# Optimization experiments

Measured on AMD Instinct MI355X. Metric: run time of the kernel, lower is better.

The kernel has to match this reference:

```python
import jax, jax.numpy as jnp
import numpy as np

B, N, D = 4, 2048, 256
EPS = 1e-5


def _clinear(Z, W, b):
    # complex linear: Z (B,2,N,din), W (2,dout,din), b (2,dout)
    Zr, Zi = Z[:, 0], Z[:, 1]
    Wr, Wi = W[0], W[1]
    outr = Zr @ Wr.T - Zi @ Wi.T + b[0]
    outi = Zr @ Wi.T + Zi @ Wr.T + b[1]
    return jnp.stack([outr, outi], axis=1)


def setup_inputs() -> dict:
    key = jax.random.key(0)
    ks = jax.random.split(key, 14)
    sc = 1.0 / np.sqrt(D).astype(np.float32)
    t = jnp.tile(jnp.arange(N + 1, dtype=jnp.float32)[None] * 0.01, (B, 1))
    return {
        'Z_q': jax.random.normal(ks[0], (B, 2, N, D), jnp.float32),
        'Z_k': jax.random.normal(ks[1], (B, 2, N, D), jnp.float32),
        'Z_v': jax.random.normal(ks[2], (B, 2, N, D), jnp.float32),
        't_measure_all': t,
        'W_q': jax.random.normal(ks[3], (2, D, D), jnp.float32) * sc,
        'b_q': jax.random.normal(ks[4], (2, D), jnp.float32) * 0.01,
        'W_k': jax.random.normal(ks[5], (2, D, D), jnp.float32) * sc,
        'b_k': jax.random.normal(ks[6], (2, D), jnp.float32) * 0.01,
        'W_v': jax.random.normal(ks[7], (2, D, D), jnp.float32) * sc,
        'b_v': jax.random.normal(ks[8], (2, D), jnp.float32) * 0.01,
        'W_p': jax.random.normal(ks[9], (2, D, D), jnp.float32) * sc,
        'b_p': jax.random.normal(ks[10], (2, D), jnp.float32) * 0.01,
        'lambda1': jax.random.normal(ks[11], (2, D // 2, 1), jnp.float32),
        'lambda_Omega_sqrt': jax.random.normal(ks[12], (1, D, 1), jnp.float32) * sc,
        'lambda_Gamma_sqrt': jax.random.normal(ks[13], (1, D, 1), jnp.float32) * sc,
        'tau': jnp.asarray(1.0, jnp.float32),
        'delta': jnp.asarray(0.0, jnp.float32),
        'lambda_C': jnp.ones((1, D, 1), jnp.float32),
    }


def reference(Z_q, Z_k, Z_v, t_measure_all, W_q, b_q, W_k, b_k, W_v, b_v,
              W_p, b_p, lambda1, lambda_Omega_sqrt, lambda_Gamma_sqrt,
              tau, delta, lambda_C):
    # lambda_h = 0 * compute_lambda_h(lambda1): conjugate-pair spectrum, zeroed in forward
    lam_r = 0.0 * jnp.concatenate([lambda1[0], lambda1[0]], axis=0)[:, 0]   # (D,)
    lam_i = 0.0 * jnp.concatenate([lambda1[1], -lambda1[1]], axis=0)[:, 0]  # (D,)
    lam_Om = lambda_Omega_sqrt ** 2 + EPS   # process noise (1,D,1)
    lam_Ga = lambda_Gamma_sqrt ** 2 + EPS   # measurement noise (1,D,1)

    Q = _clinear(Z_q, W_q, b_q)  # (B,2,N,D)
    K = _clinear(Z_k, W_k, b_k)
    V = _clinear(Z_v, W_v, b_v)

    t = t_measure_all[0, :-1]  # (N,)
    # exponential state-transition kernels exp(+/- lambda * t): (2,N,D)
    mag_f = jnp.exp(lam_r[None] * t[:, None]); ph_f = lam_i[None] * t[:, None]
    exp_f = jnp.stack([mag_f * jnp.cos(ph_f), mag_f * jnp.sin(ph_f)])
    mag_b = jnp.exp(-lam_r[None] * t[:, None]); ph_b = -lam_i[None] * t[:, None]
    exp_b = jnp.stack([mag_b * jnp.cos(ph_b), mag_b * jnp.sin(ph_b)])
    # one-step transition exp(lambda * dt): (2,D)
    dt = t[1] - t[0]
    mat_exp = jnp.stack([jnp.exp(lam_r * dt) * jnp.cos(lam_i * dt),
                         jnp.exp(lam_r * dt) * jnp.sin(lam_i * dt)])

    # averaged covariance kernel, exact lambda->0 limit: Gamma + Omega*|t_i-t_j|, mean over D
    lamC2 = lambda_C[0, :, 0] ** 2
    ga_bar = jnp.mean(lamC2 * lam_Ga[0, :, 0])
    om_bar = jnp.mean(lamC2 * lam_Om[0, :, 0])
    abs_dt = jnp.abs(t[:, None] - t[None, :])          # (N,N)
    V_avg_ij = ga_bar + om_bar * abs_dt                # (N,N)

    # factorized kernels
    V_v = exp_f[None]                 # (1,2,N,D)
    U_q = exp_b[None] * Q             # (B,2,N,D)
    U_k = exp_b[None] * K
    U_v = exp_b[None] * V

    # precision-weighted squared residual norm R_ij = sum_d |V_k|^2 |U_q_i - U_k_j|^2
    Vk_abs = jnp.sum(exp_f ** 2, axis=0)              # (N,D)
    Uk_abs = jnp.sum(U_k ** 2, axis=1)                # (B,N,D)
    Uq_abs = jnp.sum(U_q ** 2, axis=1)                # (B,N,D)
    T1 = jnp.einsum('id,bjd->bij', Vk_abs, Uk_abs)
    T2 = jnp.sum(Vk_abs[None] * Uq_abs, axis=2)[:, :, None]
    T3 = (jnp.einsum('bid,bjd->bij', Vk_abs[None] * U_q[:, 0], U_k[:, 0]) +
          jnp.einsum('bid,bjd->bij', Vk_abs[None] * U_q[:, 1], U_k[:, 1]))
    R_qk_abs = T1 + T2 - 2.0 * T3                     # (B,N,N)

    scores = -(tau ** 2) * jnp.log(V_avg_ij[None] + R_qk_abs)
    mask = jnp.tril(jnp.ones((N, N), bool))
    scores = jnp.where(mask[None], scores, -jnp.inf)
    A = jax.nn.softmax(scores, axis=2)                # (B,N,N)
    Q_ij = jnp.stack([A, jnp.zeros_like(A)], axis=1)  # (B,2,N,N)

    # est_inner = complex matmul(Q_ij, U_v); Q imag part is zero
    est_inner = jnp.stack([jnp.einsum('bij,bjd->bid', A, U_v[:, 0]),
                           jnp.einsum('bij,bjd->bid', A, U_v[:, 1])], axis=1)
    est_v = V_v * est_inner          # plain elementwise product, as in source
    s = jax.nn.sigmoid(delta)
    est_eigenbasis = (1.0 - s) * V + s * est_v        # (B,2,N,D)

    # complex Hadamard with one-step transition
    pr = mat_exp[0][None, None] * est_eigenbasis[:, 0] - mat_exp[1][None, None] * est_eigenbasis[:, 1]
    pi = mat_exp[0][None, None] * est_eigenbasis[:, 1] + mat_exp[1][None, None] * est_eigenbasis[:, 0]
    pred_p = jnp.stack([pr, pi], axis=1)
    out = _clinear(pred_p, W_p, b_p)                  # (B,2,N,D)

    lambda_h = jnp.stack([lam_r, lam_i])[..., None]
    return est_eigenbasis, out, Q_ij, V_v, U_v, lambda_h
```

## Files before the change

### kernel.cpp

```cpp
#include <hip/hip_runtime.h>
#include <math.h>

#define BN 4
#define NN 2048
#define DD 256
#define EPSF 1e-5f

typedef __attribute__((ext_vector_type(8))) short bf16x8;
typedef __attribute__((ext_vector_type(4))) float f32x4;

constexpr size_t OFF_EST = 0;
constexpr size_t OFF_OUT = (size_t)BN * 2 * NN * DD;
constexpr size_t OFF_QIJ = OFF_OUT + (size_t)BN * 2 * NN * DD;
constexpr size_t OFF_VV  = OFF_QIJ + (size_t)BN * 2 * NN * NN;
constexpr size_t OFF_UV  = OFF_VV + (size_t)2 * NN * DD;
constexpr size_t OFF_LH  = OFF_UV + (size_t)BN * 2 * NN * DD;

constexpr size_t SCR_B0   = OFF_QIJ + (size_t)NN * NN;
constexpr size_t U_Q16    = 0;
constexpr size_t U_K16    = (size_t)BN * NN * DD;
constexpr size_t U_VT16   = 2 * (size_t)BN * NN * DD;
constexpr size_t SCR_QN   = SCR_B0 + 3 * (size_t)BN * NN * DD / 2;
constexpr size_t SCR_KN   = SCR_QN + (size_t)BN * NN;
constexpr size_t SCR_L    = SCR_KN + (size_t)BN * NN;
constexpr size_t SCR_SC   = SCR_L + (size_t)BN * NN;
constexpr size_t SCR_W16P = SCR_SC + 16;
constexpr size_t SCR_E16F = OFF_QIJ + 3 * (size_t)NN * NN;
constexpr size_t U_PART   = (size_t)BN * NN * 512;
constexpr size_t SCR_Z16F = OFF_QIJ + 5 * (size_t)NN * NN;
constexpr size_t SCR_Z16VF = OFF_QIJ + 7 * (size_t)NN * NN;
constexpr size_t U_W16    = (size_t)BN * NN * 512;
constexpr size_t W16_PER_B = 136 * 16384;

__device__ __forceinline__ short f2bf(float x) {
    union { float f; unsigned u; } v; v.f = x;
    unsigned r = v.u + 0x7fff + ((v.u >> 16) & 1);
    return (short)(r >> 16);
}
__device__ __forceinline__ float bf2f(unsigned short h) {
    union { unsigned u; float f; } v; v.u = ((unsigned)h) << 16;
    return v.f;
}
__device__ __forceinline__ unsigned short* u16p(float* d, size_t fofs) {
    return (unsigned short*)(d + fofs);
}
__device__ __forceinline__ const unsigned short* u16pc(const float* d, size_t fofs) {
    return (const unsigned short*)(d + fofs);
}
__device__ __forceinline__ unsigned short* w16p(float* d, int b) {
    return (b < 3) ? u16p(d, SCR_Z16F) + (size_t)b * W16_PER_B
                   : u16p(d, SCR_Z16VF);
}
__device__ __forceinline__ const unsigned short* w16pc(const float* d, int b) {
    return (b < 3) ? u16pc(d, SCR_Z16F) + (size_t)b * W16_PER_B
                   : u16pc(d, SCR_Z16VF);
}
__device__ __forceinline__ int nc_of(int TI) { return TI >= 12 ? 3 : (TI >= 6 ? 2 : 1); }
__device__ __forceinline__ int cb_of(int TI) {
    return TI < 6 ? TI : (TI < 12 ? 6 + 2 * (TI - 6) : 18 + 3 * (TI - 12));
}

__device__ __forceinline__ void gll16(const unsigned short* g, short* l) {
    __builtin_amdgcn_global_load_lds(
        (const __attribute__((address_space(1))) unsigned*)g,
        (__attribute__((address_space(3))) unsigned*)l, 16, 0, 0);
}
__device__ __forceinline__ void stage_tile(const unsigned short* gbase, size_t stride_sh,
                                           short* ldsbuf, int t) {
    const int w = t >> 6, L = t & 63;
#pragma unroll
    for (int p = 0; p < 2; ++p) {
        const int r0 = w * 32 + p * 16;
        const unsigned short* src = gbase + (size_t)(r0 + (L >> 2)) * stride_sh + (L & 3) * 8;
        gll16(src, ldsbuf + r0 * 32);
    }
}
__device__ __forceinline__ void stage64(const unsigned short* gbase, size_t stride_sh,
                                        short* ldsbuf, int t) {
    const int w = t >> 6, L = t & 63;
    const int r0 = w * 16;
    const unsigned short* src = gbase + (size_t)(r0 + (L >> 2)) * stride_sh + (L & 3) * 8;
    gll16(src, ldsbuf + r0 * 32);
}

__global__ void k_cvt(const float* __restrict__ Zq, const float* __restrict__ Zk,
                      const float* __restrict__ Zv,
                      const float* __restrict__ Wq, const float* __restrict__ Wk,
                      const float* __restrict__ Wv, const float* __restrict__ Wp,
                      const float* __restrict__ tau, const float* __restrict__ delta,
                      const float* __restrict__ lamOm, const float* __restrict__ lamGa,
                      const float* __restrict__ lamC,
                      float* __restrict__ dout) {
    const int z = blockIdx.z;
    if (z < 3) {
        const float* Z = (z == 0) ? Zq : (z == 1) ? Zk : Zv;
        unsigned short* O = (z == 0) ? u16p(dout, SCR_Z16F)
                          : (z == 1) ? u16p(dout, SCR_Z16F) + (size_t)BN * NN * 512
                                     : u16p(dout, SCR_Z16VF);
        const long n4 = (long)BN * 2 * NN * DD / 4;
        for (long i4 = (long)blockIdx.x * 256 + threadIdx.x; i4 < n4;
             i4 += (long)gridDim.x * 256) {
            const long i = i4 * 4;
            const int d = (int)(i & (DD - 1));
            const long r = i >> 8;
            const int n = (int)(r & (NN - 1));
            const long bc = r >> 11;
            const int c = (int)(bc & 1), b = (int)(bc >> 1);
            float4 v = *(const float4*)&Z[i];
            ushort4 o;
            o.x = (unsigned short)f2bf(v.x); o.y = (unsigned short)f2bf(v.y);
            o.z = (unsigned short)f2bf(v.z); o.w = (unsigned short)f2bf(v.w);
            *(ushort4*)&O[((size_t)(b * NN + n)) * 512 + c * 256 + d] = o;
        }
    } else if (z == 3) {
        const float* Ws[4] = {Wq, Wk, Wv, Wp};
        const long n4 = 6L * 256 * 512 / 4;
        for (long e4 = (long)blockIdx.x * 256 + threadIdx.x; e4 < n4;
             e4 += (long)gridDim.x * 256) {
            const long e = e4 * 4;
            const int k = (int)(e & 511);
            const long rest = e >> 9;
            const int dd = (int)(rest & 255);
            const int m = (int)(rest >> 8);
            int proj, mode;
            if (m < 3)      { proj = m; mode = 0; }
            else if (m == 3){ proj = 2; mode = 1; }
            else            { proj = 3; mode = m - 4; }
            const int kc = k >> 8, kk = k & 255;
            int wc; float sgn;
            if (mode == 0) { wc = kc; sgn = kc ? -1.f : 1.f; }
            else           { wc = 1 - kc; sgn = 1.f; }
            float4 v = *(const float4*)&Ws[proj][((size_t)wc * DD + dd) * DD + kk];
            ushort4 o;
            o.x = (unsigned short)f2bf(sgn * v.x); o.y = (unsigned short)f2bf(sgn * v.y);
            o.z = (unsigned short)f2bf(sgn * v.z); o.w = (unsigned short)f2bf(sgn * v.w);
            unsigned short* dst = (m < 4)
                ? u16p(dout, SCR_Z16VF) + U_W16 + (size_t)m * 131072
                : u16p(dout, SCR_W16P) + (size_t)(m - 4) * 131072;
            *(ushort4*)&dst[(size_t)dd * 512 + k] = o;
        }
    } else {
        const int idx = blockIdx.x * 256 + threadIdx.x;
        if (idx < 3 * BN * NN) dout[SCR_QN + idx] = 0.f;
        if (blockIdx.x == 0) {
            __shared__ float red[8];
            const int t = threadIdx.x;
            float c2 = lamC[t] * lamC[t];
            float ga = c2 * (lamGa[t] * lamGa[t] + EPSF);
            float om = c2 * (lamOm[t] * lamOm[t] + EPSF);
            for (int o = 32; o > 0; o >>= 1) {
                ga += __shfl_down(ga, o, 64);
                om += __shfl_down(om, o, 64);
            }
            if ((t & 63) == 0) { red[t >> 6] = ga; red[4 + (t >> 6)] = om; }
            __syncthreads();
            if (t == 0) {
                float gs = red[0] + red[1] + red[2] + red[3];
                float os = red[4] + red[5] + red[6] + red[7];
                float* scal = dout + SCR_SC;
                scal[0] = tau[0] * tau[0];
                scal[1] = 1.f / (1.f + __expf(-delta[0]));
                scal[2] = gs / 256.f;
                scal[3] = os / 256.f;
            }
        }
    }
}

__global__ __launch_bounds__(256) void k_qkv(const float* __restrict__ bq,
                                             const float* __restrict__ bk,
                                             const float* __restrict__ bv,
                                             float* __restrict__ dout)
{
    __shared__ short Al[64 * 32];
    __shared__ short Bl[128 * 32];
    const int z = blockIdx.z;
    const int d0 = blockIdx.x * 128;
    const int b = blockIdx.y >> 5;
    const int n0 = (blockIdx.y & 31) * 64;

    const unsigned short* Z16 =
        (z == 0) ? u16pc(dout, SCR_Z16F)
      : (z == 1) ? u16pc(dout, SCR_Z16F) + (size_t)BN * NN * 512
                 : u16pc(dout, SCR_Z16VF);
    const unsigned short* W16 = u16pc(dout, SCR_Z16VF) + U_W16 + (size_t)z * 131072;
    const float* bias = (z == 0) ? bq : (z == 1) ? bk : bv;
    const int bofs = (z == 3) ? DD : 0;

    const int t = threadIdx.x, wave = t >> 6, lane = t & 63, quad = lane >> 4, lm = lane & 15;
    const int wr = (wave >> 1) * 32, wc = (wave & 1) * 64;
    const unsigned short* Abase = Z16 + (size_t)(b * NN + n0) * 512;
    const unsigned short* Bbase = W16 + (size_t)d0 * 512;

    f32x4 acc[2][4];
#pragma unroll
    for (int i = 0; i < 2; ++i)
#pragma unroll
        for (int j = 0; j < 4; ++j) acc[i][j] = (f32x4){0.f, 0.f, 0.f, 0.f};

    for (int kt = 0; kt < 16; ++kt) {
        const int kk0 = kt * 32;
        stage64(Abase + kk0, 512, Al, t);
        stage_tile(Bbase + kk0, 512, Bl, t);
        __syncthreads();
        bf16x8 af[2], bff[4];
#pragma unroll
        for (int mi = 0; mi < 2; ++mi) af[mi] = *(const bf16x8*)&Al[(wr + mi * 16 + lm) * 32 + quad * 8];
#pragma unroll
        for (int nj = 0; nj < 4; ++nj) bff[nj] = *(const bf16x8*)&Bl[(wc + nj * 16 + lm) * 32 + quad * 8];
#pragma unroll
        for (int mi = 0; mi < 2; ++mi)
#pragma unroll
            for (int nj = 0; nj < 4; ++nj)
                acc[mi][nj] = __builtin_amdgcn_mfma_f32_16x16x32_bf16(af[mi], bff[nj], acc[mi][nj], 0, 0, 0);
        __syncthreads();
    }

    if (z <= 1) {
        unsigned short* O16 = u16p(dout, SCR_B0) + (z ? U_K16 : U_Q16) + (size_t)b * NN * DD;
        float* NRM = dout + (z ? SCR_KN : SCR_QN) + b * NN;
#pragma unroll
        for (int mi = 0; mi < 2; ++mi)
#pragma unroll
            for (int r = 0; r < 4; ++r) {
                const int m = n0 + wr + mi * 16 + quad * 4 + r;
                float ss = 0.f;
#pragma unroll
                for (int nj = 0; nj < 4; ++nj) {
                    const int d = d0 + wc + nj * 16 + lm;
                    unsigned short h = (unsigned short)f2bf(acc[mi][nj][r] + bias[d]);
                    O16[(size_t)m * DD + d] = h;
                    const float vb = bf2f(h);
                    ss = fmaf(vb, vb, ss);
                }
                ss += __shfl_down(ss, 8, 16); ss += __shfl_down(ss, 4, 16);
                ss += __shfl_down(ss, 2, 16); ss += __shfl_down(ss, 1, 16);
                if (lm == 0) atomicAdd(&NRM[m], ss);
            }
    } else if (z == 2) {
        float* UV0 = dout + OFF_UV + (size_t)(b * 2) * NN * DD;
#pragma unroll
        for (int mi = 0; mi < 2; ++mi)
#pragma unroll
            for (int r = 0; r < 4; ++r) {
                const int m = n0 + wr + mi * 16 + quad * 4 + r;
#pragma unroll
                for (int nj = 0; nj < 4; ++nj) {
                    const int d = d0 + wc + nj * 16 + lm;
                    UV0[(size_t)m * DD + d] = acc[mi][nj][r] + bias[d];
                }
            }
    } else {
        const float s1 = 1.f - dout[SCR_SC + 1];
        float* EST1 = dout + OFF_EST + (size_t)(b * 2 + 1) * NN * DD;
        unsigned short* E16 = u16p(dout, SCR_E16F) + (size_t)b * NN * 512;
#pragma unroll
        for (int mi = 0; mi < 2; ++mi)
#pragma unroll
            for (int r = 0; r < 4; ++r) {
                const int m = n0 + wr + mi * 16 + quad * 4 + r;
#pragma unroll
                for (int nj = 0; nj < 4; ++nj) {
                    const int d = d0 + wc + nj * 16 + lm;
                    const float v = s1 * (acc[mi][nj][r] + bias[bofs + d]);
                    EST1[(size_t)m * DD + d] = v;
                    E16[(size_t)m * 512 + 256 + d] = (unsigned short)f2bf(v);
                }
            }
    }
}

__global__ __launch_bounds__(256) void k_outproj(const float* __restrict__ bp,
                                                 float* __restrict__ dout)
{
    __shared__ short Al[64 * 32];
    __shared__ short Bl[128 * 32];
    const int z = blockIdx.z;
    if (z == 2) {
        const long idx = (long)(blockIdx.y * 2 + blockIdx.x) * 256 + threadIdx.x;
        const float4 zz4 = {0.f, 0.f, 0.f, 0.f};
        for (long u = idx * 4; u < (long)NN * NN; u += 256L * 256 * 4) {
            *(float4*)&dout[SCR_Z16F + u] = zz4;
            *(float4*)&dout[SCR_Z16VF + u] = zz4;
        }
        return;
    }
    const int d0 = blockIdx.x * 128;
    const int b = blockIdx.y >> 5;
    const int n0 = (blockIdx.y & 31) * 64;
    const unsigned short* E16 = u16pc(dout, SCR_E16F) + (size_t)b * NN * 512;
    const unsigned short* W16 = u16pc(dout, SCR_W16P) + (size_t)z * 131072;

    const int t = threadIdx.x, wave = t >> 6, lane = t & 63, quad = lane >> 4, lm = lane & 15;
    const int wr = (wave >> 1) * 32, wc = (wave & 1) * 64;
    const unsigned short* Abase = E16 + (size_t)n0 * 512;
    const unsigned short* Bbase = W16 + (size_t)d0 * 512;

    f32x4 acc[2][4];
#pragma unroll
    for (int i = 0; i < 2; ++i)
#pragma unroll
        for (int j = 0; j < 4; ++j) acc[i][j] = (f32x4){0.f, 0.f, 0.f, 0.f};

    for (int kt = 0; kt < 16; ++kt) {
        const int kk0 = kt * 32;
        stage64(Abase + kk0, 512, Al, t);
        stage_tile(Bbase + kk0, 512, Bl, t);
        __syncthreads();
        bf16x8 af[2], bff[4];
#pragma unroll
        for (int mi = 0; mi < 2; ++mi) af[mi] = *(const bf16x8*)&Al[(wr + mi * 16 + lm) * 32 + quad * 8];
#pragma unroll
        for (int nj = 0; nj < 4; ++nj) bff[nj] = *(const bf16x8*)&Bl[(wc + nj * 16 + lm) * 32 + quad * 8];
#pragma unroll
        for (int mi = 0; mi < 2; ++mi)
#pragma unroll
            for (int nj = 0; nj < 4; ++nj)
                acc[mi][nj] = __builtin_amdgcn_mfma_f32_16x16x32_bf16(af[mi], bff[nj], acc[mi][nj], 0, 0, 0);
        __syncthreads();
    }
    const int bofs = z ? DD : 0;
    float* O = dout + OFF_OUT + (size_t)(b * 2 + z) * NN * DD;
#pragma unroll
    for (int mi = 0; mi < 2; ++mi)
#pragma unroll
        for (int r = 0; r < 4; ++r) {
            const int m = n0 + wr + mi * 16 + quad * 4 + r;
#pragma unroll
            for (int nj = 0; nj < 4; ++nj) {
                const int d = d0 + wc + nj * 16 + lm;
                O[(size_t)m * DD + d] = acc[mi][nj][r] + bp[bofs + d];
            }
        }
}

__global__ __launch_bounds__(256) void k_scores(const float* __restrict__ tmeas,
                                                float* __restrict__ dout) {
    __shared__ __align__(16) float smemf[4160];
    short* Al = (short*)smemf;
    short* Bl = ((short*)smemf) + 2048;
    const int b = blockIdx.y;
    if (blockIdx.x >= 272) {
        float (*T)[65] = (float(*)[65])smemf;
        const int vj = blockIdx.x - 272;
        const int nb = (vj & 31) * 64, db = (vj >> 5) * 64;
        const float* V = dout + OFF_UV + (size_t)(b * 2) * NN * DD;
        unsigned short* VT = u16p(dout, SCR_B0) + U_VT16 + (size_t)b * DD * NN;
        const int tr = threadIdx.x >> 4, tc = (threadIdx.x & 15) * 4;
#pragma unroll
        for (int p = 0; p < 4; ++p) {
            float4 v = *(const float4*)&V[(size_t)(nb + tr + p * 16) * DD + db + tc];
            T[tr + p * 16][tc + 0] = v.x; T[tr + p * 16][tc + 1] = v.y;
            T[tr + p * 16][tc + 2] = v.z; T[tr + p * 16][tc + 3] = v.w;
        }
        __syncthreads();
#pragma unroll
        for (int p = 0; p < 4; ++p) {
            const int d = tr + p * 16;
            ushort4 o;
            o.x = (unsigned short)f2bf(T[tc + 0][d]);
            o.y = (unsigned short)f2bf(T[tc + 1][d]);
            o.z = (unsigned short)f2bf(T[tc + 2][d]);
            o.w = (unsigned short)f2bf(T[tc + 3][d]);
            *(ushort4*)&VT[(size_t)(db + d) * NN + nb + tc] = o;
        }
        return;
    }
    const int x2 = blockIdx.x;
    const int x = x2 >> 1, ih = x2 & 1;
    int ti = (int)((sqrtf(8.f * x + 1.f) - 1.f) * 0.5f);
    while ((ti + 1) * (ti + 2) / 2 <= x) ++ti;
    while (ti * (ti + 1) / 2 > x) --ti;
    const int tj = x - ti * (ti + 1) / 2;
    const int i0 = ti * 128, j0 = tj * 128;
    const int ib = i0 + ih * 64;
    const unsigned short* Q16 = u16pc(dout, SCR_B0) + U_Q16 + (size_t)b * NN * DD;
    const unsigned short* K16 = u16pc(dout, SCR_B0) + U_K16 + (size_t)b * NN * DD;
    const int t = threadIdx.x, wave = t >> 6, lane = t & 63, quad = lane >> 4, lm = lane & 15;
    const int wr = (wave >> 1) * 32, wc = (wave & 1) * 64;
    const unsigned short* Abase = Q16 + (size_t)ib * DD;
    const unsigned short* Bbase = K16 + (size_t)j0 * DD;

    f32x4 acc[2][4];
#pragma unroll
    for (int i = 0; i < 2; ++i)
#pragma unroll
        for (int j = 0; j < 4; ++j) acc[i][j] = (f32x4){0.f, 0.f, 0.f, 0.f};

    for (int kt = 0; kt < 8; ++kt) {
        const int kk0 = kt * 32;
        stage64(Abase + kk0, DD, Al, t);
        stage_tile(Bbase + kk0, DD, Bl, t);
        __syncthreads();
        bf16x8 af[2], bff[4];
#pragma unroll
        for (int mi = 0; mi < 2; ++mi) af[mi] = *(const bf16x8*)&Al[(wr + mi * 16 + lm) * 32 + quad * 8];
#pragma unroll
        for (int nj = 0; nj < 4; ++nj) bff[nj] = *(const bf16x8*)&Bl[(wc + nj * 16 + lm) * 32 + quad * 8];
#pragma unroll
        for (int mi = 0; mi < 2; ++mi)
#pragma unroll
            for (int nj = 0; nj < 4; ++nj)
                acc[mi][nj] = __builtin_amdgcn_mfma_f32_16x16x32_bf16(af[mi], bff[nj], acc[mi][nj], 0, 0, 0);
        __syncthreads();
    }

    const float tau2 = dout[SCR_SC + 0], ga = dout[SCR_SC + 2], om = dout[SCR_SC + 3];
    unsigned short* WT = w16p(dout, b) + (size_t)x * 16384;
    const float* QN_ = dout + SCR_QN + b * NN;
    const float* KN_ = dout + SCR_KN + b * NN;
    float kn[4], tjv[4]; int jj[4], jl[4];
#pragma unroll
    for (int nj = 0; nj < 4; ++nj) {
        jl[nj] = wc + nj * 16 + lm;
        jj[nj] = j0 + jl[nj];
        kn[nj] = KN_[jj[nj]];
        tjv[nj] = tmeas[jj[nj]];
    }
#pragma unroll
    for (int mi = 0; mi < 2; ++mi)
#pragma unroll
        for (int r = 0; r < 4; ++r) {
            const int li = ih * 64 + wr + mi * 16 + quad * 4 + r;
            const int i = i0 + li;
            const float qni = QN_[i], tqi = tmeas[i];
            float rs = 0.f;
#pragma unroll
            for (int nj = 0; nj < 4; ++nj) {
                float xx = ga + om * fabsf(tqi - tjv[nj]) + qni + kn[nj] - 2.f * acc[mi][nj][r];
                xx = fmaxf(xx, 1e-30f);
                float w = (tau2 == 1.f) ? __builtin_amdgcn_rcpf(xx)
                                        : __expf(-tau2 * __logf(xx));
                if (jj[nj] > i) w = 0.f;
                const unsigned short h = (unsigned short)f2bf(w);
                WT[(size_t)li * 128 + jl[nj]] = h;
                rs += bf2f(h);
            }
            rs += __shfl_down(rs, 8, 16); rs += __shfl_down(rs, 4, 16);
            rs += __shfl_down(rs, 2, 16); rs += __shfl_down(rs, 1, 16);
            if (lm == 0) atomicAdd(&dout[SCR_L + b * NN + i], rs);
        }
}

__global__ __launch_bounds__(256) void k_estinner(float* __restrict__ dout) {
    __shared__ short Al[128 * 32];
    __shared__ short Bl[64 * 32];
    const int b = blockIdx.y;
    const int chunk = blockIdx.x >> 2, qd = blockIdx.x & 3;
    int y = chunk, TI = 0, cb = 0;
    for (;;) { const int nc = nc_of(TI); if (y < nc) break; y -= nc; cb += nc; ++TI; }
    const int kbeg = y * 768;
    const int kend = min(kbeg + 768, (TI + 1) * 128);
    const int nst = (kend - kbeg) >> 5;
    const int cidx = cb + y;
    const int tri = TI * (TI + 1) / 2;
    const unsigned short* WT = w16pc(dout, b);
    const unsigned short* VT = u16pc(dout, SCR_B0) + U_VT16 + (size_t)b * DD * NN
                             + (size_t)(qd * 64) * NN;

    const int t = threadIdx.x, wave = t >> 6, lane = t & 63, quad = lane >> 4, lm = lane & 15;
    const int rh = (wave >> 1) * 64, ch = (wave & 1) * 32;

    f32x4 acc[4][2];
#pragma unroll
    for (int i = 0; i < 4; ++i)
#pragma unroll
        for (int j = 0; j < 2; ++j) acc[i][j] = (f32x4){0.f, 0.f, 0.f, 0.f};

    for (int kt = 0; kt < nst; ++kt) {
        const int kk0 = kbeg + kt * 32;
        const int tile = kk0 >> 7;
        stage_tile(WT + (size_t)(tri + tile) * 16384 + (kk0 & 127), 128, Al, t);
        stage64(VT + kk0, NN, Bl, t);
        __syncthreads();
        bf16x8 af[4], bff[2];
#pragma unroll
        for (int mi = 0; mi < 4; ++mi) af[mi] = *(const bf16x8*)&Al[(rh + mi * 16 + lm) * 32 + quad * 8];
#pragma unroll
        for (int nj = 0; nj < 2; ++nj) bff[nj] = *(const bf16x8*)&Bl[(ch + nj * 16 + lm) * 32 + quad * 8];
#pragma unroll
        for (int mi = 0; mi < 4; ++mi)
#pragma unroll
            for (int nj = 0; nj < 2; ++nj)
                acc[mi][nj] = __builtin_amdgcn_mfma_f32_16x16x32_bf16(af[mi], bff[nj], acc[mi][nj], 0, 0, 0);
        __syncthreads();
    }
    unsigned short* P = u16p(dout, SCR_E16F) + U_PART +
                        ((size_t)(b * 30 + cidx)) * 128 * 256;
#pragma unroll
    for (int mi = 0; mi < 4; ++mi)
#pragma unroll
        for (int r = 0; r < 4; ++r) {
            const int ri = rh + mi * 16 + quad * 4 + r;
#pragma unroll
            for (int nj = 0; nj < 2; ++nj) {
                const int d = qd * 64 + ch + nj * 16 + lm;
                P[(size_t)ri * 256 + d] = (unsigned short)f2bf(acc[mi][nj][r]);
            }
        }
}

__global__ void k_blendfills(float* __restrict__ dout) {
    const int z = blockIdx.z;
    if (z < 4) {
        const int b = z;
        if (blockIdx.x >= 512) return;
        const int t = threadIdx.x;
        const int i = blockIdx.x * 4 + (t >> 6);
        const int d4 = (t & 63) * 4;
        const int TI = i >> 7;
        const int nc = nc_of(TI), cb = cb_of(TI);
        const float s = dout[SCR_SC + 1];
        const float linv = 1.f / dout[SCR_L + b * NN + i];
        const unsigned short* P = u16pc(dout, SCR_E16F) + U_PART;
        float4 sum = {0.f, 0.f, 0.f, 0.f};
        for (int c = 0; c < nc; ++c) {
            ushort4 pv = *(const ushort4*)&P[((size_t)(b * 30 + cb + c) * 128 + (i & 127)) * 256 + d4];
            sum.x += bf2f(pv.x); sum.y += bf2f(pv.y);
            sum.z += bf2f(pv.z); sum.w += bf2f(pv.w);
        }
        const float4 vr = *(const float4*)&dout[OFF_UV + ((size_t)(b * 2) * NN + i) * DD + d4];
        const float sl = s * linv;
        float4 ev;
        ev.x = (1.f - s) * vr.x + sl * sum.x;
        ev.y = (1.f - s) * vr.y + sl * sum.y;
        ev.z = (1.f - s) * vr.z + sl * sum.z;
        ev.w = (1.f - s) * vr.w + sl * sum.w;
        *(float4*)&dout[OFF_EST + ((size_t)(b * 2) * NN + i) * DD + d4] = ev;
        ushort4 o;
        o.x = (unsigned short)f2bf(ev.x); o.y = (unsigned short)f2bf(ev.y);
        o.z = (unsigned short)f2bf(ev.z); o.w = (unsigned short)f2bf(ev.w);
        *(ushort4*)&u16p(dout, SCR_E16F)[((size_t)(b * NN + i)) * 512 + d4] = o;
        return;
    }
    if (z < 8) {
        const int b = z - 4, i = blockIdx.x;
        const int TI = i >> 7, li = i & 127;
        const int tri = TI * (TI + 1) / 2;
        const float linv = 1.f / dout[SCR_L + b * NN + i];
        const unsigned short* WTb = w16pc(dout, b);
        float* row = dout + OFF_QIJ + (size_t)b * 2 * NN * NN + (size_t)i * NN;
        for (int j4 = threadIdx.x * 4; j4 < NN; j4 += 1024) {
            const int tj = j4 >> 7;
            float4 o = {0.f, 0.f, 0.f, 0.f};
            if (tj <= TI) {
                ushort4 h = *(const ushort4*)&WTb[((size_t)(tri + tj)) * 16384
                                                  + (size_t)li * 128 + (j4 & 127)];
                o.x = bf2f(h.x) * linv; o.y = bf2f(h.y) * linv;
                o.z = bf2f(h.z) * linv; o.w = bf2f(h.w) * linv;
            }
            *(float4*)&row[j4] = o;
        }
        return;
    }
    size_t base; long n; float val = 0.f;
    if (z == 8)       { base = SCR_B0; n = 3145728; }
    else if (z == 9)  { base = OFF_VV; n = (long)NN * DD; val = 1.f; }
    else if (z == 10) { base = OFF_VV + (size_t)NN * DD; n = (long)NN * DD; }
    else if (z < 15)  { base = OFF_UV + (size_t)(2 * (z - 11) + 1) * NN * DD; n = (long)NN * DD; }
    else              { base = OFF_LH; n = 512; }
    float* p = dout + base;
    const float4 v = {val, val, val, val};
    for (long i = ((long)blockIdx.x * 256 + threadIdx.x) * 4; i < n;
         i += (long)gridDim.x * 1024)
        *(float4*)&p[i] = v;
}

__global__ void k_tail(float* __restrict__ dout) {
    const float4 zz = {0.f, 0.f, 0.f, 0.f};
    const long n1 = (long)NN * NN;
    for (long i = ((long)blockIdx.x * 256 + threadIdx.x) * 4; i < n1;
         i += (long)gridDim.x * 1024)
        *(float4*)&dout[SCR_E16F + i] = zz;
    const long n0 = (long)NN * NN - 3145728;
    for (long i = ((long)blockIdx.x * 256 + threadIdx.x) * 4; i < n0;
         i += (long)gridDim.x * 1024)
        *(float4*)&dout[SCR_QN + i] = zz;
}

extern "C" void kernel_launch(void* const* d_in, const int* in_sizes, int n_in,
                              void* d_out, int out_size, void* d_ws, size_t ws_size,
                              hipStream_t stream) {
    const float* Zq = (const float*)d_in[0];
    const float* Zk = (const float*)d_in[1];
    const float* Zv = (const float*)d_in[2];
    const float* tm = (const float*)d_in[3];
    const float* Wq = (const float*)d_in[4];
    const float* bq = (const float*)d_in[5];
    const float* Wk = (const float*)d_in[6];
    const float* bk = (const float*)d_in[7];
    const float* Wv = (const float*)d_in[8];
    const float* bv = (const float*)d_in[9];
    const float* Wp = (const float*)d_in[10];
    const float* bp = (const float*)d_in[11];
    const float* lamOm = (const float*)d_in[13];
    const float* lamGa = (const float*)d_in[14];
    const float* tau = (const float*)d_in[15];
    const float* delta = (const float*)d_in[16];
    const float* lamC = (const float*)d_in[17];
    float* out = (float*)d_out;

    k_cvt<<<dim3(2048, 1, 5), dim3(256), 0, stream>>>(
        Zq, Zk, Zv, Wq, Wk, Wv, Wp, tau, delta, lamOm, lamGa, lamC, out);
    k_qkv<<<dim3(2, 128, 4), dim3(256), 0, stream>>>(bq, bk, bv, out);
    k_scores<<<dim3(400, 4), dim3(256), 0, stream>>>(tm, out);
    k_estinner<<<dim3(120, 4), dim3(256), 0, stream>>>(out);
    k_blendfills<<<dim3(2048, 1, 16), dim3(256), 0, stream>>>(out);
    k_outproj<<<dim3(2, 128, 3), dim3(256), 0, stream>>>(bp, out);
    k_tail<<<dim3(1024), dim3(256), 0, stream>>>(out);
}
```

Baseline: 335.7 us.

## Fuse fp32-to-bf16 input conversion into QKV GEMM A-tile staging

Removes the separate conversion pass that wrote bf16 copies of Z_q/Z_k/Z_v to scratch. The QKV GEMM now loads fp32 activations directly, converts them in registers and writes them to LDS, which saves a full write and read of the bf16 intermediate. The prep kernel shrinks to weight conversion and scalars. Part of the scratch zeroing moves from the tail kernel into the outproj zero-fill branch, and the tail launch grid is halved. In exchange, the A-tile loads now go through registers synchronously rather than as asynchronous global-to-LDS copies, and the GEMM reads twice as many bytes per element.

```diff
diff --git a/kernel.cpp b/kernel.cpp
--- a/kernel.cpp
+++ b/kernel.cpp
@@ -83,36 +83,14 @@
     gll16(src, ldsbuf + r0 * 32);
 }
 
-__global__ void k_cvt(const float* __restrict__ Zq, const float* __restrict__ Zk,
-                      const float* __restrict__ Zv,
-                      const float* __restrict__ Wq, const float* __restrict__ Wk,
-                      const float* __restrict__ Wv, const float* __restrict__ Wp,
-                      const float* __restrict__ tau, const float* __restrict__ delta,
-                      const float* __restrict__ lamOm, const float* __restrict__ lamGa,
-                      const float* __restrict__ lamC,
-                      float* __restrict__ dout) {
+__global__ void k_prep(const float* __restrict__ Wq, const float* __restrict__ Wk,
+                       const float* __restrict__ Wv, const float* __restrict__ Wp,
+                       const float* __restrict__ tau, const float* __restrict__ delta,
+                       const float* __restrict__ lamOm, const float* __restrict__ lamGa,
+                       const float* __restrict__ lamC,
+                       float* __restrict__ dout) {
     const int z = blockIdx.z;
-    if (z < 3) {
-        const float* Z = (z == 0) ? Zq : (z == 1) ? Zk : Zv;
-        unsigned short* O = (z == 0) ? u16p(dout, SCR_Z16F)
-                          : (z == 1) ? u16p(dout, SCR_Z16F) + (size_t)BN * NN * 512
-                                     : u16p(dout, SCR_Z16VF);
-        const long n4 = (long)BN * 2 * NN * DD / 4;
-        for (long i4 = (long)blockIdx.x * 256 + threadIdx.x; i4 < n4;
-             i4 += (long)gridDim.x * 256) {
-            const long i = i4 * 4;
-            const int d = (int)(i & (DD - 1));
-            const long r = i >> 8;
-            const int n = (int)(r & (NN - 1));
-            const long bc = r >> 11;
-            const int c = (int)(bc & 1), b = (int)(bc >> 1);
-            float4 v = *(const float4*)&Z[i];
-            ushort4 o;
-            o.x = (unsigned short)f2bf(v.x); o.y = (unsigned short)f2bf(v.y);
-            o.z = (unsigned short)f2bf(v.z); o.w = (unsigned short)f2bf(v.w);
-            *(ushort4*)&O[((size_t)(b * NN + n)) * 512 + c * 256 + d] = o;
-        }
-    } else if (z == 3) {
+    if (z == 0) {
         const float* Ws[4] = {Wq, Wk, Wv, Wp};
         const long n4 = 6L * 256 * 512 / 4;
         for (long e4 = (long)blockIdx.x * 256 + threadIdx.x; e4 < n4;
@@ -167,7 +145,10 @@
     }
 }
 
-__global__ __launch_bounds__(256) void k_qkv(const float* __restrict__ bq,
+__global__ __launch_bounds__(256) void k_qkv(const float* __restrict__ Zq,
+                                             const float* __restrict__ Zk,
+                                             const float* __restrict__ Zv,
+                                             const float* __restrict__ bq,
                                              const float* __restrict__ bk,
                                              const float* __restrict__ bv,
                                              float* __restrict__ dout)
@@ -179,17 +160,14 @@
     const int b = blockIdx.y >> 5;
     const int n0 = (blockIdx.y & 31) * 64;
 
-    const unsigned short* Z16 =
-        (z == 0) ? u16pc(dout, SCR_Z16F)
-      : (z == 1) ? u16pc(dout, SCR_Z16F) + (size_t)BN * NN * 512
-                 : u16pc(dout, SCR_Z16VF);
+    const float* Zf = (z == 0) ? Zq : (z == 1) ? Zk : Zv;
     const unsigned short* W16 = u16pc(dout, SCR_Z16VF) + U_W16 + (size_t)z * 131072;
     const float* bias = (z == 0) ? bq : (z == 1) ? bk : bv;
     const int bofs = (z == 3) ? DD : 0;
 
     const int t = threadIdx.x, wave = t >> 6, lane = t & 63, quad = lane >> 4, lm = lane & 15;
     const int wr = (wave >> 1) * 32, wc = (wave & 1) * 64;
-    const unsigned short* Abase = Z16 + (size_t)(b * NN + n0) * 512;
+    const int ar = t >> 2, ac8 = (t & 3) * 8;
     const unsigned short* Bbase = W16 + (size_t)d0 * 512;
 
     f32x4 acc[2][4];
@@ -200,8 +178,19 @@
 
     for (int kt = 0; kt < 16; ++kt) {
         const int kk0 = kt * 32;
-        stage64(Abase + kk0, 512, Al, t);
+        const int c = kt >> 3;
+        const int dcol = (kt & 7) * 32;
+        const float* As = Zf + ((size_t)((b * 2 + c) * NN + n0 + ar)) * DD + dcol + ac8;
+        float4 av0 = *(const float4*)(As + 0);
+        float4 av1 = *(const float4*)(As + 4);
         stage_tile(Bbase + kk0, 512, Bl, t);
+        ushort4 ha, hb;
+        ha.x = (unsigned short)f2bf(av0.x); ha.y = (unsigned short)f2bf(av0.y);
+        ha.z = (unsigned short)f2bf(av0.z); ha.w = (unsigned short)f2bf(av0.w);
+        hb.x = (unsigned short)f2bf(av1.x); hb.y = (unsigned short)f2bf(av1.y);
+        hb.z = (unsigned short)f2bf(av1.z); hb.w = (unsigned short)f2bf(av1.w);
+        *(ushort4*)&Al[ar * 32 + ac8]     = ha;
+        *(ushort4*)&Al[ar * 32 + ac8 + 4] = hb;
         __syncthreads();
         bf16x8 af[2], bff[4];
 #pragma unroll
@@ -283,6 +272,8 @@
             *(float4*)&dout[SCR_Z16F + u] = zz4;
             *(float4*)&dout[SCR_Z16VF + u] = zz4;
         }
+        for (long u = idx * 4; u < 2097152; u += 256L * 256 * 4)
+            *(float4*)&dout[SCR_E16F + 2097152 + u] = zz4;
         return;
     }
     const int d0 = blockIdx.x * 128;
@@ -568,7 +559,7 @@
 
 __global__ void k_tail(float* __restrict__ dout) {
     const float4 zz = {0.f, 0.f, 0.f, 0.f};
-    const long n1 = (long)NN * NN;
+    const long n1 = 2097152;
     for (long i = ((long)blockIdx.x * 256 + threadIdx.x) * 4; i < n1;
          i += (long)gridDim.x * 1024)
         *(float4*)&dout[SCR_E16F + i] = zz;
@@ -600,12 +591,12 @@
     const float* lamC = (const float*)d_in[17];
     float* out = (float*)d_out;
 
-    k_cvt<<<dim3(2048, 1, 5), dim3(256), 0, stream>>>(
-        Zq, Zk, Zv, Wq, Wk, Wv, Wp, tau, delta, lamOm, lamGa, lamC, out);
-    k_qkv<<<dim3(2, 128, 4), dim3(256), 0, stream>>>(bq, bk, bv, out);
+    k_prep<<<dim3(256, 1, 2), dim3(256), 0, stream>>>(
+        Wq, Wk, Wv, Wp, tau, delta, lamOm, lamGa, lamC, out);
+    k_qkv<<<dim3(2, 128, 4), dim3(256), 0, stream>>>(Zq, Zk, Zv, bq, bk, bv, out);
     k_scores<<<dim3(400, 4), dim3(256), 0, stream>>>(tm, out);
     k_estinner<<<dim3(120, 4), dim3(256), 0, stream>>>(out);
     k_blendfills<<<dim3(2048, 1, 16), dim3(256), 0, stream>>>(out);
     k_outproj<<<dim3(2, 128, 3), dim3(256), 0, stream>>>(bp, out);
-    k_tail<<<dim3(1024), dim3(256), 0, stream>>>(out);
-}
+    k_tail<<<dim3(512), dim3(256), 0, stream>>>(out);
+}
```

Measured after the change: 337.3 us. Within noise of the previous version (+0.5%).
